# Kernel tuning notes

Hardware: AMD Instinct MI355X
Metric: run time of the kernel (lower is better)

The kernel has to match this reference:

```python
import jax, jax.numpy as jnp
import numpy as np
import math

D_MODEL = 1024
N_HEADS = 8
HEAD_DIM = D_MODEL // N_HEADS
N_CLASSES = 2


def setup_inputs() -> dict:
    key = jax.random.key(0)
    ks = jax.random.split(key, 12)
    s = 1.0 / math.sqrt(D_MODEL)
    return {
        "x": jax.random.normal(ks[0], (8192, D_MODEL), dtype=jnp.float32),
        "class_token": jax.random.normal(ks[1], (1, 1, D_MODEL), dtype=jnp.float32),
        "Wq": jax.random.normal(ks[2], (D_MODEL, D_MODEL), dtype=jnp.float32) * s,
        "bq": jnp.zeros((D_MODEL,), jnp.float32),
        "Wk": jax.random.normal(ks[3], (D_MODEL, D_MODEL), dtype=jnp.float32) * s,
        "bk": jnp.zeros((D_MODEL,), jnp.float32),
        "Wv": jax.random.normal(ks[4], (D_MODEL, D_MODEL), dtype=jnp.float32) * s,
        "bv": jnp.zeros((D_MODEL,), jnp.float32),
        "Wo": jax.random.normal(ks[5], (D_MODEL, D_MODEL), dtype=jnp.float32) * s,
        "bo": jnp.zeros((D_MODEL,), jnp.float32),
        "Wc": jax.random.normal(ks[6], (N_CLASSES, D_MODEL), dtype=jnp.float32) * s,
        "bc": jnp.zeros((N_CLASSES,), jnp.float32),
    }


def reference(x, class_token, Wq, bq, Wk, bk, Wv, bv, Wo, bo, Wc, bc):
    # Prepend class token: [T, D] with T = N_patches + 1 (batch size is 1)
    tokens = jnp.concatenate([class_token.reshape(1, D_MODEL), x], axis=0)
    T = tokens.shape[0]
    scale = 1.0 / math.sqrt(HEAD_DIM)

    def heads(W, b):
        return (tokens @ W.T + b).reshape(T, N_HEADS, HEAD_DIM).transpose(1, 0, 2)

    q = heads(Wq, bq)  # [H, T, hd]
    k = heads(Wk, bk)
    v = heads(Wv, bv)

    scores = jnp.einsum("htd,hsd->hts", q, k) * scale  # [H, T, T]
    probs = jax.nn.softmax(scores, axis=-1)
    attn_out = jnp.einsum("hts,hsd->htd", probs, v)  # [H, T, hd]

    # MIL attention weights: class-token row, over patches, head-averaged
    A = probs[:, 0, 1:].mean(axis=0)[None, :]  # [1, N_patches]

    out = attn_out.transpose(1, 0, 2).reshape(T, D_MODEL) @ Wo.T + bo  # [T, D]
    cls_out = out[0:1]  # [1, D]

    logits = cls_out @ Wc.T + bc  # [1, n_classes]
    y_probs = jax.nn.softmax(logits, axis=1)

    m = jnp.argmax(y_probs.reshape(-1))
    row = m // N_CLASSES
    Y_hat = (m % N_CLASSES)[None]  # [1]
    top_instance = jnp.take(logits, row, axis=0)[None]  # [1, n_classes]
    Y_prob = jnp.take(y_probs, row, axis=0)[None]  # [1, n_classes]

    return top_instance, Y_prob, Y_hat, y_probs, A
```

## Files before the change

### kernel.cpp

```cpp
#include <hip/hip_runtime.h>
#include <math.h>

#define D 1024
#define NH 8
#define T 8193

#define OFF_QCLS  0
#define OFF_EP    1024
#define OFF_W     17408
#define OFF_G     25600
#define OFF_CH    41984
#define OFF_CONST 41992
#define OFF_L     42000
#define OFF_PLOG  44048
#define OFF_SCT   48144

static __device__ __forceinline__ float wred(float v) {
    #pragma unroll
    for (int m = 32; m; m >>= 1) v += __shfl_xor(v, m, 64);
    return v;
}

#define DPPADD(v, ctrl) \
    ((v) + __int_as_float(__builtin_amdgcn_update_dpp( \
        0, __float_as_int(v), (ctrl), 0xf, 0xf, true)))

static __device__ __forceinline__ float wave_total(float v) {
    v = DPPADD(v, 0x111);
    v = DPPADD(v, 0x112);
    v = DPPADD(v, 0x114);
    v = DPPADD(v, 0x118);
    v = DPPADD(v, 0x142);
    v = DPPADD(v, 0x143);
    return __int_as_float(__builtin_amdgcn_readlane(__float_as_int(v), 63));
}

__global__ __launch_bounds__(1024) void k1(const float* __restrict__ Wq,
                                           const float* __restrict__ bq,
                                           const float* __restrict__ ct,
                                           const float* __restrict__ Wc,
                                           const float* __restrict__ Wo,
                                           float* __restrict__ ws) {
    __shared__ float red[16];
    __shared__ float er[4][2][256];
    const int b = blockIdx.x, t = threadIdx.x;
    const int w = t >> 6, lane = t & 63;
    if (b < 256) {
        int grp = t >> 8, f4 = t & 255;
        int r = b * 4 + grp;
        const float4* wr = (const float4*)(Wq + (size_t)r * D);
        const float4* cv = (const float4*)ct;
        float4 a = wr[f4], c = cv[f4];
        float v = a.x*c.x + a.y*c.y + a.z*c.z + a.w*c.w;
        v = wred(v);
        if (lane == 0) red[w] = v;
        __syncthreads();
        if (t < 4)
            ws[OFF_QCLS + b*4 + t] = red[4*t]+red[4*t+1]+red[4*t+2]+red[4*t+3] + bq[b*4 + t];
    } else {
        int idx = b - 256;
        int p = idx >> 2, jq = idx & 3;
        int layer = t >> 8, jl = t & 255;
        int j = jq * 256 + jl;
        int i0 = p * 128 + layer * 32;
        const float* wo = Wo + (size_t)i0 * D + j;
        float a0 = 0.f, a1 = 0.f;
        #pragma unroll 8
        for (int i = 0; i < 32; ++i) {
            float r = wo[(size_t)i * D];
            a0 += Wc[i0 + i] * r;
            a1 += Wc[D + i0 + i] * r;
        }
        er[layer][0][jl] = a0;
        er[layer][1][jl] = a1;
        __syncthreads();
        if (t < 512) {
            int c = t >> 8, jl2 = t & 255;
            ws[OFF_EP + p*2048 + c*1024 + jq*256 + jl2] =
                er[0][c][jl2] + er[1][c][jl2] + er[2][c][jl2] + er[3][c][jl2];
        }
    }
}

__global__ __launch_bounds__(1024) void k2(const float* __restrict__ Wk,
                                           const float* __restrict__ bk,
                                           const float* __restrict__ Wv,
                                           const float* __restrict__ Wc,
                                           const float* __restrict__ bo,
                                           const float* __restrict__ bv,
                                           const float* __restrict__ bc,
                                           float* __restrict__ ws) {
    __shared__ float qh[128];
    __shared__ float el[2][128];
    __shared__ float lr[4][2][256];
    __shared__ float red[32];
    const int b = blockIdx.x, t = threadIdx.x;
    const int w = t >> 6, lane = t & 63;
    if (b < 32) {
        int h = b >> 2, jq = b & 3;
        if (t < 128) qh[t] = ws[OFF_QCLS + h*128 + t];
        __syncthreads();
        int layer = t >> 8, jl = t & 255;
        int j = jq * 256 + jl, d0 = layer * 32;
        const float* wk = Wk + (size_t)(h*128 + d0) * D + j;
        float acc = 0.f;
        #pragma unroll 8
        for (int d = 0; d < 32; ++d) acc += qh[d0 + d] * wk[(size_t)d * D];
        lr[layer][0][jl] = acc;
        __syncthreads();
        if (t < 256)
            ws[OFF_W + h*1024 + jq*256 + t] = lr[0][0][t]+lr[1][0][t]+lr[2][0][t]+lr[3][0][t];
    } else if (b < 64) {
        int hb = b - 32, h = hb >> 2, jq = hb & 3;
        if (t < 256) {
            int c = t >> 7, r = t & 127;
            float s = 0.f;
            #pragma unroll
            for (int p = 0; p < 8; ++p) s += ws[OFF_EP + p*2048 + c*1024 + h*128 + r];
            el[c][r] = s;
        }
        __syncthreads();
        int layer = t >> 8, jl = t & 255;
        int j = jq * 256 + jl, r0 = layer * 32;
        const float* wv = Wv + (size_t)(h*128 + r0) * D + j;
        float a0 = 0.f, a1 = 0.f;
        #pragma unroll 8
        for (int r = 0; r < 32; ++r) {
            float xv = wv[(size_t)r * D];
            a0 += el[0][r0 + r] * xv;
            a1 += el[1][r0 + r] * xv;
        }
        lr[layer][0][jl] = a0;
        lr[layer][1][jl] = a1;
        __syncthreads();
        if (t < 512) {
            int c = t >> 8, jl2 = t & 255;
            ws[OFF_G + c*8192 + h*1024 + jq*256 + jl2] =
                lr[0][c][jl2] + lr[1][c][jl2] + lr[2][c][jl2] + lr[3][c][jl2];
        }
    } else if (b == 64) {
        int h = t >> 7, d = t & 127;
        float v = ws[OFF_QCLS + h*128 + d] * bk[h*128 + d];
        v = wred(v);
        if (lane == 0) red[w] = v;
        __syncthreads();
        if (t < 8) ws[OFF_CH + t] = red[2*t] + red[2*t+1];
    } else {
        float e0 = 0.f, e1 = 0.f;
        #pragma unroll
        for (int p = 0; p < 8; ++p) {
            e0 += ws[OFF_EP + p*2048 + t];
            e1 += ws[OFF_EP + p*2048 + 1024 + t];
        }
        float v0 = Wc[t]*bo[t] + e0*bv[t];
        float v1 = Wc[D + t]*bo[t] + e1*bv[t];
        v0 = wred(v0); v1 = wred(v1);
        if (lane == 0) { red[w] = v0; red[16 + w] = v1; }
        __syncthreads();
        if (t == 0) {
            float a0 = 0.f, a1 = 0.f;
            #pragma unroll
            for (int i = 0; i < 16; ++i) { a0 += red[i]; a1 += red[16 + i]; }
            ws[OFF_CONST + 0] = a0 + bc[0];
            ws[OFF_CONST + 1] = a1 + bc[1];
        }
    }
}

__global__ __launch_bounds__(512, 2) void k3(const float* __restrict__ x,
                                             const float* __restrict__ ct,
                                             float* __restrict__ ws) {
    __shared__ float stash[33 * D];
    __shared__ float pe[33][8];
    __shared__ float plred[8][8];
    const int b = blockIdx.x, t = threadIdx.x;
    const int w = t >> 6, lane = t & 63;

    float4 wreg[8][4];
    const float4* wg4 = (const float4*)(ws + OFF_W);
    #pragma unroll
    for (int h = 0; h < 8; ++h)
        #pragma unroll
        for (int j = 0; j < 4; ++j)
            wreg[h][j] = wg4[h * 256 + j * 64 + lane];
    float chv[8];
    #pragma unroll
    for (int h = 0; h < 8; ++h) chv[h] = ws[OFF_CH + h];

    const int ntok_blk = (b == 255) ? 33 : 32;
    const bool tail = (b == 255 && w == 7);
    const int ntok_w = tail ? 5 : 4;
    for (int i = 0; i < ntok_w; ++i) {
        int k = (i < 4) ? (w * 4 + i) : 32;
        int s = b * 32 + k;
        const float* row = (s == 0) ? ct : (x + (size_t)(s - 1) * D);
        float* dst = stash + k * D;
        #pragma unroll
        for (int q = 0; q < 4; ++q)
            __builtin_amdgcn_global_load_lds(
                (const __attribute__((address_space(1))) unsigned int*)(row + q * 256 + lane * 4),
                (__attribute__((address_space(3))) unsigned int*)(dst + q * 256),
                16, 0, 0);
    }

    const float scale = 0.08838834764831845f;
    auto compute = [&](int k) {
        int s = b * 32 + k;
        const float4* tk = (const float4*)(stash + k * D);
        float4 t0 = tk[lane], t1 = tk[64 + lane], t2 = tk[128 + lane], t3 = tk[192 + lane];
        float pv[8];
        #pragma unroll
        for (int h = 0; h < 8; ++h) {
            float4 w0 = wreg[h][0], w1 = wreg[h][1], w2 = wreg[h][2], w3 = wreg[h][3];
            float v = w0.x*t0.x + w0.y*t0.y + w0.z*t0.z + w0.w*t0.w
                    + w1.x*t1.x + w1.y*t1.y + w1.z*t1.z + w1.w*t1.w
                    + w2.x*t2.x + w2.y*t2.y + w2.z*t2.z + w2.w*t2.w
                    + w3.x*t3.x + w3.y*t3.y + w3.z*t3.z + w3.w*t3.w;
            v = wave_total(v);
            pv[h] = __expf(scale * (v + chv[h]));
        }
        if (lane == 0) {
            float4* sct = (float4*)(ws + OFF_SCT);
            sct[s * 2]     = make_float4(pv[0], pv[1], pv[2], pv[3]);
            sct[s * 2 + 1] = make_float4(pv[4], pv[5], pv[6], pv[7]);
            *(float4*)&pe[k][0] = make_float4(pv[0], pv[1], pv[2], pv[3]);
            *(float4*)&pe[k][4] = make_float4(pv[4], pv[5], pv[6], pv[7]);
        }
    };

    if (!tail) {
        __builtin_amdgcn_s_waitcnt(0x0f7c); compute(w*4 + 0);
        __builtin_amdgcn_s_waitcnt(0x0f78); compute(w*4 + 1);
        __builtin_amdgcn_s_waitcnt(0x0f74); compute(w*4 + 2);
        __builtin_amdgcn_s_waitcnt(0x0f70); compute(w*4 + 3);
    } else {
        __builtin_amdgcn_s_waitcnt(0x0f70);
        for (int i = 0; i < 5; ++i) compute((i < 4) ? (w*4 + i) : 32);
    }
    __syncthreads();

    if (t < 8) {
        float s = 0.f;
        for (int k = 0; k < ntok_blk; ++k) s += pe[k][t];
        ws[OFF_L + b * 8 + t] = s;
    }

    const int f4 = t & 255, half = t >> 8;
    const float4* st4 = (const float4*)stash;
    float4 acc0 = {0,0,0,0}, acc1 = {0,0,0,0}, acc2 = {0,0,0,0}, acc3 = {0,0,0,0};
    for (int k = 0; k < ntok_blk; ++k) {
        float4 tv = st4[k * 256 + f4];
        float4 pv = *(const float4*)&pe[k][half * 4];
        acc0.x += pv.x*tv.x; acc0.y += pv.x*tv.y; acc0.z += pv.x*tv.z; acc0.w += pv.x*tv.w;
        acc1.x += pv.y*tv.x; acc1.y += pv.y*tv.y; acc1.z += pv.y*tv.z; acc1.w += pv.y*tv.w;
        acc2.x += pv.z*tv.x; acc2.y += pv.z*tv.y; acc2.z += pv.z*tv.z; acc2.w += pv.z*tv.w;
        acc3.x += pv.w*tv.x; acc3.y += pv.w*tv.y; acc3.z += pv.w*tv.z; acc3.w += pv.w*tv.w;
    }

    const float4* G4 = (const float4*)(ws + OFF_G);
    float pl[8];
    #pragma unroll
    for (int c = 0; c < 2; ++c) {
        float4 g0 = G4[c*2048 + (half*4 + 0)*256 + f4];
        float4 g1 = G4[c*2048 + (half*4 + 1)*256 + f4];
        float4 g2 = G4[c*2048 + (half*4 + 2)*256 + f4];
        float4 g3 = G4[c*2048 + (half*4 + 3)*256 + f4];
        pl[c*4+0] = g0.x*acc0.x + g0.y*acc0.y + g0.z*acc0.z + g0.w*acc0.w;
        pl[c*4+1] = g1.x*acc1.x + g1.y*acc1.y + g1.z*acc1.z + g1.w*acc1.w;
        pl[c*4+2] = g2.x*acc2.x + g2.y*acc2.y + g2.z*acc2.z + g2.w*acc2.w;
        pl[c*4+3] = g3.x*acc3.x + g3.y*acc3.y + g3.z*acc3.z + g3.w*acc3.w;
    }
    #pragma unroll
    for (int v = 0; v < 8; ++v) pl[v] = wave_total(pl[v]);
    if (lane == 0)
        #pragma unroll
        for (int v = 0; v < 8; ++v) plred[w][v] = pl[v];
    __syncthreads();
    if (t < 16) {
        int c = t >> 3, hh = t & 7;
        int wb = (hh < 4) ? 0 : 4, vi = c * 4 + (hh & 3);
        ws[OFF_PLOG + b*16 + t] =
            plred[wb][vi] + plred[wb+1][vi] + plred[wb+2][vi] + plred[wb+3][vi];
    }
}

__global__ __launch_bounds__(256) void k4(float* __restrict__ out,
                                          float* __restrict__ ws) {
    __shared__ float lp[32][8];
    __shared__ float rlh[8];
    __shared__ float r2[8];
    const int b = blockIdx.x, t = threadIdx.x;

    {
        int seg = t >> 3, h = t & 7;
        float s = 0.f;
        for (int pb = seg; pb < 256; pb += 32) s += ws[OFF_L + pb*8 + h];
        lp[seg][h] = s;
    }
    __syncthreads();
    if (t < 8) {
        float s = 0.f;
        #pragma unroll
        for (int i = 0; i < 32; ++i) s += lp[i][t];
        rlh[t] = 1.f / s;
    }
    __syncthreads();

    if (t < 32) {
        int s_ = b * 32 + t + 1;
        const float4* sct = (const float4*)(ws + OFF_SCT);
        float4 pa = sct[s_ * 2], pb4 = sct[s_ * 2 + 1];
        float sum = pa.x*rlh[0] + pa.y*rlh[1] + pa.z*rlh[2] + pa.w*rlh[3]
                  + pb4.x*rlh[4] + pb4.y*rlh[5] + pb4.z*rlh[6] + pb4.w*rlh[7];
        out[6 + s_] = sum * 0.125f;
    }

    if (b == 0) {
        float v0 = 0.f, v1 = 0.f;
        for (int idx = t; idx < 4096; idx += 256) {
            float val = ws[OFF_PLOG + idx];
            int rem = idx & 15;
            float z = val * rlh[rem & 7];
            if ((rem >> 3) == 0) v0 += z; else v1 += z;
        }
        v0 = wred(v0); v1 = wred(v1);
        if ((t & 63) == 0) { r2[t >> 6] = v0; r2[4 + (t >> 6)] = v1; }
        __syncthreads();
        if (t == 0) {
            float l0 = r2[0]+r2[1]+r2[2]+r2[3] + ws[OFF_CONST + 0];
            float l1 = r2[4]+r2[5]+r2[6]+r2[7] + ws[OFF_CONST + 1];
            float mx = fmaxf(l0, l1);
            float e0 = __expf(l0 - mx), e1 = __expf(l1 - mx);
            float inv = 1.f / (e0 + e1);
            float p0 = e0 * inv, p1 = e1 * inv;
            int am = (p1 > p0) ? 1 : 0;
            out[0] = l0; out[1] = l1;
            out[2] = p0; out[3] = p1;
            out[4] = (float)am;
            out[5] = p0; out[6] = p1;
        }
    }
}

extern "C" void kernel_launch(void* const* d_in, const int* in_sizes, int n_in,
                              void* d_out, int out_size, void* d_ws, size_t ws_size,
                              hipStream_t stream) {
    const float* x  = (const float*)d_in[0];
    const float* ct = (const float*)d_in[1];
    const float* Wq = (const float*)d_in[2];
    const float* bq = (const float*)d_in[3];
    const float* Wk = (const float*)d_in[4];
    const float* bk = (const float*)d_in[5];
    const float* Wv = (const float*)d_in[6];
    const float* bv = (const float*)d_in[7];
    const float* Wo = (const float*)d_in[8];
    const float* bo = (const float*)d_in[9];
    const float* Wc = (const float*)d_in[10];
    const float* bc = (const float*)d_in[11];
    float* out = (float*)d_out;
    float* ws  = (float*)d_ws;

    k1<<<dim3(288), dim3(1024), 0, stream>>>(Wq, bq, ct, Wc, Wo, ws);
    k2<<<dim3(66),  dim3(1024), 0, stream>>>(Wk, bk, Wv, Wc, bo, bv, bc, ws);
    k3<<<dim3(256), dim3(512),  0, stream>>>(x, ct, ws);
    k4<<<dim3(256), dim3(256),  0, stream>>>(out, ws);
}
```

Measured before the change: 125.1 us.

## Halve tokens per block in k3, split heads across wave pairs, double k1 Wo partials

The main pass kernel now uses 512 blocks of 16 tokens instead of 256 blocks of 32. Each pair of waves splits the 8 heads in half, so every wave holds only 4 heads of score weights in registers, and the launch bound allows 4 blocks per CU. The Wo·Wc projection in k1 is split into 16 partial slabs instead of 8 to use more blocks, and the downstream reductions are resized to match. In exchange, the staged per-token score computation is replaced by a single wait-all barrier, which gives up overlap between loads and compute, and there are twice as many partial results to reduce in k4.

After: 129.4 us. +3.4%, slower.

```diff
diff --git a/kernel.cpp b/kernel.cpp
--- a/kernel.cpp
+++ b/kernel.cpp
@@ -7,13 +7,13 @@
 
 #define OFF_QCLS  0
 #define OFF_EP    1024
-#define OFF_W     17408
-#define OFF_G     25600
-#define OFF_CH    41984
-#define OFF_CONST 41992
-#define OFF_L     42000
-#define OFF_PLOG  44048
-#define OFF_SCT   48144
+#define OFF_W     33792
+#define OFF_G     41984
+#define OFF_CH    58368
+#define OFF_CONST 58376
+#define OFF_L     58384
+#define OFF_PLOG  62480
+#define OFF_SCT   70672
 
 static __device__ __forceinline__ float wred(float v) {
     #pragma unroll
@@ -62,11 +62,11 @@
         int p = idx >> 2, jq = idx & 3;
         int layer = t >> 8, jl = t & 255;
         int j = jq * 256 + jl;
-        int i0 = p * 128 + layer * 32;
+        int i0 = p * 64 + layer * 16;
         const float* wo = Wo + (size_t)i0 * D + j;
         float a0 = 0.f, a1 = 0.f;
         #pragma unroll 8
-        for (int i = 0; i < 32; ++i) {
+        for (int i = 0; i < 16; ++i) {
             float r = wo[(size_t)i * D];
             a0 += Wc[i0 + i] * r;
             a1 += Wc[D + i0 + i] * r;
@@ -116,7 +116,7 @@
             int c = t >> 7, r = t & 127;
             float s = 0.f;
             #pragma unroll
-            for (int p = 0; p < 8; ++p) s += ws[OFF_EP + p*2048 + c*1024 + h*128 + r];
+            for (int p = 0; p < 16; ++p) s += ws[OFF_EP + p*2048 + c*1024 + h*128 + r];
             el[c][r] = s;
         }
         __syncthreads();
@@ -148,7 +148,7 @@
     } else {
         float e0 = 0.f, e1 = 0.f;
         #pragma unroll
-        for (int p = 0; p < 8; ++p) {
+        for (int p = 0; p < 16; ++p) {
             e0 += ws[OFF_EP + p*2048 + t];
             e1 += ws[OFF_EP + p*2048 + 1024 + t];
         }
@@ -167,32 +167,31 @@
     }
 }
 
-__global__ __launch_bounds__(512, 2) void k3(const float* __restrict__ x,
+__global__ __launch_bounds__(512, 4) void k3(const float* __restrict__ x,
                                              const float* __restrict__ ct,
                                              float* __restrict__ ws) {
-    __shared__ float stash[33 * D];
-    __shared__ float pe[33][8];
+    __shared__ float stash[17 * D];
+    __shared__ float pe[17][8];
     __shared__ float plred[8][8];
     const int b = blockIdx.x, t = threadIdx.x;
     const int w = t >> 6, lane = t & 63;
-
-    float4 wreg[8][4];
+    const int hh = w & 1, tg = w >> 1;
+
+    float4 wreg[4][4];
     const float4* wg4 = (const float4*)(ws + OFF_W);
     #pragma unroll
-    for (int h = 0; h < 8; ++h)
+    for (int e = 0; e < 4; ++e)
         #pragma unroll
         for (int j = 0; j < 4; ++j)
-            wreg[h][j] = wg4[h * 256 + j * 64 + lane];
-    float chv[8];
-    #pragma unroll
-    for (int h = 0; h < 8; ++h) chv[h] = ws[OFF_CH + h];
-
-    const int ntok_blk = (b == 255) ? 33 : 32;
-    const bool tail = (b == 255 && w == 7);
-    const int ntok_w = tail ? 5 : 4;
-    for (int i = 0; i < ntok_w; ++i) {
-        int k = (i < 4) ? (w * 4 + i) : 32;
-        int s = b * 32 + k;
+            wreg[e][j] = wg4[(hh*4 + e) * 256 + j * 64 + lane];
+    float chv[4];
+    #pragma unroll
+    for (int e = 0; e < 4; ++e) chv[e] = ws[OFF_CH + hh*4 + e];
+
+    const int ntok = (b == 511) ? 17 : 16;
+    {
+        int k = tg * 2 + hh;
+        int s = b * 16 + k;
         const float* row = (s == 0) ? ct : (x + (size_t)(s - 1) * D);
         float* dst = stash + k * D;
         #pragma unroll
@@ -201,56 +200,58 @@
                 (const __attribute__((address_space(1))) unsigned int*)(row + q * 256 + lane * 4),
                 (__attribute__((address_space(3))) unsigned int*)(dst + q * 256),
                 16, 0, 0);
-    }
+        if (b == 511 && w == 14) {
+            const float* row2 = x + (size_t)(8192 - 1) * D;
+            float* dst2 = stash + 16 * D;
+            #pragma unroll
+            for (int q = 0; q < 4; ++q)
+                __builtin_amdgcn_global_load_lds(
+                    (const __attribute__((address_space(1))) unsigned int*)(row2 + q * 256 + lane * 4),
+                    (__attribute__((address_space(3))) unsigned int*)(dst2 + q * 256),
+                    16, 0, 0);
+        }
+    }
+    __builtin_amdgcn_s_waitcnt(0x0f70);
+    __syncthreads();
 
     const float scale = 0.08838834764831845f;
-    auto compute = [&](int k) {
-        int s = b * 32 + k;
+    const int extra = (b == 511 && tg == 7) ? 1 : 0;
+    for (int i = 0; i < 2 + extra; ++i) {
+        int k = (i < 2) ? (tg * 2 + i) : 16;
+        int s = b * 16 + k;
         const float4* tk = (const float4*)(stash + k * D);
         float4 t0 = tk[lane], t1 = tk[64 + lane], t2 = tk[128 + lane], t3 = tk[192 + lane];
-        float pv[8];
-        #pragma unroll
-        for (int h = 0; h < 8; ++h) {
-            float4 w0 = wreg[h][0], w1 = wreg[h][1], w2 = wreg[h][2], w3 = wreg[h][3];
+        float pv[4];
+        #pragma unroll
+        for (int e = 0; e < 4; ++e) {
+            float4 w0 = wreg[e][0], w1 = wreg[e][1], w2 = wreg[e][2], w3 = wreg[e][3];
             float v = w0.x*t0.x + w0.y*t0.y + w0.z*t0.z + w0.w*t0.w
                     + w1.x*t1.x + w1.y*t1.y + w1.z*t1.z + w1.w*t1.w
                     + w2.x*t2.x + w2.y*t2.y + w2.z*t2.z + w2.w*t2.w
                     + w3.x*t3.x + w3.y*t3.y + w3.z*t3.z + w3.w*t3.w;
             v = wave_total(v);
-            pv[h] = __expf(scale * (v + chv[h]));
+            pv[e] = __expf(scale * (v + chv[e]));
         }
         if (lane == 0) {
-            float4* sct = (float4*)(ws + OFF_SCT);
-            sct[s * 2]     = make_float4(pv[0], pv[1], pv[2], pv[3]);
-            sct[s * 2 + 1] = make_float4(pv[4], pv[5], pv[6], pv[7]);
-            *(float4*)&pe[k][0] = make_float4(pv[0], pv[1], pv[2], pv[3]);
-            *(float4*)&pe[k][4] = make_float4(pv[4], pv[5], pv[6], pv[7]);
-        }
-    };
-
-    if (!tail) {
-        __builtin_amdgcn_s_waitcnt(0x0f7c); compute(w*4 + 0);
-        __builtin_amdgcn_s_waitcnt(0x0f78); compute(w*4 + 1);
-        __builtin_amdgcn_s_waitcnt(0x0f74); compute(w*4 + 2);
-        __builtin_amdgcn_s_waitcnt(0x0f70); compute(w*4 + 3);
-    } else {
-        __builtin_amdgcn_s_waitcnt(0x0f70);
-        for (int i = 0; i < 5; ++i) compute((i < 4) ? (w*4 + i) : 32);
+            float4 p4 = make_float4(pv[0], pv[1], pv[2], pv[3]);
+            ((float4*)(ws + OFF_SCT))[s * 2 + hh] = p4;
+            *(float4*)&pe[k][hh * 4] = p4;
+        }
     }
     __syncthreads();
 
     if (t < 8) {
         float s = 0.f;
-        for (int k = 0; k < ntok_blk; ++k) s += pe[k][t];
+        for (int k = 0; k < ntok; ++k) s += pe[k][t];
         ws[OFF_L + b * 8 + t] = s;
     }
 
-    const int f4 = t & 255, half = t >> 8;
+    const int f4 = t & 255, hp = t >> 8;
     const float4* st4 = (const float4*)stash;
     float4 acc0 = {0,0,0,0}, acc1 = {0,0,0,0}, acc2 = {0,0,0,0}, acc3 = {0,0,0,0};
-    for (int k = 0; k < ntok_blk; ++k) {
+    for (int k = 0; k < ntok; ++k) {
         float4 tv = st4[k * 256 + f4];
-        float4 pv = *(const float4*)&pe[k][half * 4];
+        float4 pv = *(const float4*)&pe[k][hp * 4];
         acc0.x += pv.x*tv.x; acc0.y += pv.x*tv.y; acc0.z += pv.x*tv.z; acc0.w += pv.x*tv.w;
         acc1.x += pv.y*tv.x; acc1.y += pv.y*tv.y; acc1.z += pv.y*tv.z; acc1.w += pv.y*tv.w;
         acc2.x += pv.z*tv.x; acc2.y += pv.z*tv.y; acc2.z += pv.z*tv.z; acc2.w += pv.z*tv.w;
@@ -261,10 +262,10 @@
     float pl[8];
     #pragma unroll
     for (int c = 0; c < 2; ++c) {
-        float4 g0 = G4[c*2048 + (half*4 + 0)*256 + f4];
-        float4 g1 = G4[c*2048 + (half*4 + 1)*256 + f4];
-        float4 g2 = G4[c*2048 + (half*4 + 2)*256 + f4];
-        float4 g3 = G4[c*2048 + (half*4 + 3)*256 + f4];
+        float4 g0 = G4[c*2048 + (hp*4 + 0)*256 + f4];
+        float4 g1 = G4[c*2048 + (hp*4 + 1)*256 + f4];
+        float4 g2 = G4[c*2048 + (hp*4 + 2)*256 + f4];
+        float4 g3 = G4[c*2048 + (hp*4 + 3)*256 + f4];
         pl[c*4+0] = g0.x*acc0.x + g0.y*acc0.y + g0.z*acc0.z + g0.w*acc0.w;
         pl[c*4+1] = g1.x*acc1.x + g1.y*acc1.y + g1.z*acc1.z + g1.w*acc1.w;
         pl[c*4+2] = g2.x*acc2.x + g2.y*acc2.y + g2.z*acc2.z + g2.w*acc2.w;
@@ -277,10 +278,10 @@
         for (int v = 0; v < 8; ++v) plred[w][v] = pl[v];
     __syncthreads();
     if (t < 16) {
-        int c = t >> 3, hh = t & 7;
-        int wb = (hh < 4) ? 0 : 4, vi = c * 4 + (hh & 3);
+        int c = t >> 3, h = t & 7;
+        int hp2 = h >> 2, vi = c * 4 + (h & 3);
         ws[OFF_PLOG + b*16 + t] =
-            plred[wb][vi] + plred[wb+1][vi] + plred[wb+2][vi] + plred[wb+3][vi];
+            plred[hp2*4][vi] + plred[hp2*4+1][vi] + plred[hp2*4+2][vi] + plred[hp2*4+3][vi];
     }
 }
 
@@ -294,7 +295,7 @@
     {
         int seg = t >> 3, h = t & 7;
         float s = 0.f;
-        for (int pb = seg; pb < 256; pb += 32) s += ws[OFF_L + pb*8 + h];
+        for (int pb = seg; pb < 512; pb += 32) s += ws[OFF_L + pb*8 + h];
         lp[seg][h] = s;
     }
     __syncthreads();
@@ -317,7 +318,7 @@
 
     if (b == 0) {
         float v0 = 0.f, v1 = 0.f;
-        for (int idx = t; idx < 4096; idx += 256) {
+        for (int idx = t; idx < 8192; idx += 256) {
             float val = ws[OFF_PLOG + idx];
             int rem = idx & 15;
             float z = val * rlh[rem & 7];
@@ -360,8 +361,8 @@
     float* out = (float*)d_out;
     float* ws  = (float*)d_ws;
 
-    k1<<<dim3(288), dim3(1024), 0, stream>>>(Wq, bq, ct, Wc, Wo, ws);
+    k1<<<dim3(320), dim3(1024), 0, stream>>>(Wq, bq, ct, Wc, Wo, ws);
     k2<<<dim3(66),  dim3(1024), 0, stream>>>(Wk, bk, Wv, Wc, bo, bv, bc, ws);
-    k3<<<dim3(256), dim3(512),  0, stream>>>(x, ct, ws);
+    k3<<<dim3(512), dim3(512),  0, stream>>>(x, ct, ws);
     k4<<<dim3(256), dim3(256),  0, stream>>>(out, ws);
 }
```
